# Kernel tuning notes

Measured on AMD Instinct MI355X. Metric: run time of the kernel, lower is better.

## Reference

```python
import jax, jax.numpy as jnp
import numpy as np

B, S, E, H = 4, 1024, 1024, 16
D = E // H  # head_dim = 64
SCALE = float(np.sqrt(D))


def setup_inputs() -> dict:
    key = jax.random.key(0)
    ks = jax.random.split(key, 12)
    lim = 1.0 / np.sqrt(E)  # torch nn.Linear default init range

    def lin(kw, kb):
        W = jax.random.uniform(kw, (E, E), jnp.float32, -lim, lim)
        b = jax.random.uniform(kb, (E,), jnp.float32, -lim, lim)
        return W, b

    W0, b0 = lin(ks[0], ks[1])
    W1, b1 = lin(ks[2], ks[3])
    W2, b2 = lin(ks[4], ks[5])
    Wv, bv = lin(ks[6], ks[7])
    Wo, bo = lin(ks[8], ks[9])
    A = jax.random.normal(ks[10], (D, D, D), jnp.float32)  # torch.randn core tensor
    x = jax.random.normal(ks[11], (B, S, E), jnp.float32)
    return {"x": x, "W0": W0, "b0": b0, "W1": W1, "b1": b1, "W2": W2, "b2": b2,
            "Wv": Wv, "bv": bv, "Wo": Wo, "bo": bo, "A": A}


def _heads(h):
    # (B,S,E) -> (B,H,S,D)
    return h.reshape(B, S, H, D).transpose(0, 2, 1, 3)


def reference(x, W0, b0, W1, b1, W2, b2, Wv, bv, Wo, bo, A):
    p0 = _heads(x @ W0.T + b0)
    p1 = _heads(x @ W1.T + b1)
    p2 = _heads(x @ W2.T + b2)
    # N=3 multilinear attention score: third projection is contracted over its
    # own sequence index k (faithful to the original einsum construction).
    logits = jnp.einsum('acd,bhia,bhjc,bhkd->bhij', A, p0, p1, p2,
                        optimize=True) / SCALE  # (B,H,S,S)
    attn = jax.nn.softmax(logits, axis=-1)  # dropout inactive (eval / p=0)
    v = _heads(x @ Wv.T + bv)
    values = jnp.einsum('bhij,bhjd->bhid', attn, v)  # (B,H,S,D)
    values = values.transpose(0, 2, 1, 3).reshape(B, S, E)
    out = values @ Wo.T + bo
    return out, attn
```

## Files before the change

kernel.cpp:

```cpp
#include <hip/hip_runtime.h>
#include <hip/hip_bf16.h>
#include <cstddef>

#define B_ 4
#define S_ 1024
#define E_ 1024
#define H_ 16
#define D_ 64
#define BH_ (B_*H_)

typedef __attribute__((ext_vector_type(8))) short short8;
typedef __attribute__((ext_vector_type(4))) float f32x4;
typedef __attribute__((ext_vector_type(4))) unsigned short us4;
typedef unsigned short u16;

__device__ inline u16 f2b(float x) {
    return __builtin_bit_cast(u16, __float2bfloat16(x));
}
__device__ inline float b2f(u16 u) {
    return __bfloat162float(__builtin_bit_cast(__hip_bfloat16, u));
}
__device__ inline void splitf(float x, u16& h, u16& l) {
    h = f2b(x); l = f2b(x - b2f(h));
}

__device__ inline void split_one(const float* __restrict__ in,
                                 u16* __restrict__ oh, u16* __restrict__ ol, int i)
{
    float4 v = ((const float4*)in)[i];
    us4 h, l;
    splitf(v.x, ((u16*)&h)[0], ((u16*)&l)[0]);
    splitf(v.y, ((u16*)&h)[1], ((u16*)&l)[1]);
    splitf(v.z, ((u16*)&h)[2], ((u16*)&l)[2]);
    splitf(v.w, ((u16*)&h)[3], ((u16*)&l)[3]);
    ((us4*)oh)[i] = h;
    ((us4*)ol)[i] = l;
}

__device__ inline void conv_one(const float* __restrict__ in,
                                u16* __restrict__ ob, int i)
{
    float4 v = ((const float4*)in)[i];
    us4 h;
    ((u16*)&h)[0] = f2b(v.x); ((u16*)&h)[1] = f2b(v.y);
    ((u16*)&h)[2] = f2b(v.z); ((u16*)&h)[3] = f2b(v.w);
    ((us4*)ob)[i] = h;
}

__global__ __launch_bounds__(256) void prep(
    const float* __restrict__ x, const float* __restrict__ W0,
    const float* __restrict__ W1, const float* __restrict__ Wv,
    const float* __restrict__ Wo, float* __restrict__ xsum_p,
    u16* __restrict__ xh, u16* __restrict__ xl,
    u16* __restrict__ w0h, u16* __restrict__ w0l,
    u16* __restrict__ w1h, u16* __restrict__ w1l,
    u16* __restrict__ wvb, u16* __restrict__ wob)
{
    int bid = blockIdx.x, tid = threadIdx.x;
    if (bid < 4096) {
        split_one(x, xh, xl, bid * 256 + tid);
    } else if (bid < 5120) {
        split_one(W0, w0h, w0l, (bid - 4096) * 256 + tid);
    } else if (bid < 6144) {
        split_one(W1, w1h, w1l, (bid - 5120) * 256 + tid);
    } else if (bid < 7168) {
        conv_one(Wv, wvb, (bid - 6144) * 256 + tid);
    } else if (bid < 8192) {
        conv_one(Wo, wob, (bid - 7168) * 256 + tid);
    } else {
        int p = bid - 8192;
        int kb = p & 3, b = (p >> 2) & 3, ch = p >> 4;
        int k = kb * 256 + tid;
        const float* base = x + ((size_t)(b * S_ + ch * 64)) * E_ + k;
        float s = 0.f;
#pragma unroll 8
        for (int j = 0; j < 64; ++j) s += base[(size_t)j * E_];
        xsum_p[(ch * 4 + b) * E_ + k] = s;
    }
}

__global__ __launch_bounds__(256) void t2k_M(
    const float* __restrict__ W2, const float* __restrict__ b2v,
    const float* __restrict__ xsum_p, const float* __restrict__ A,
    u16* __restrict__ MTh, u16* __restrict__ MTl)
{
    int h = blockIdx.x, b = blockIdx.y, tid = threadIdx.x;
    __shared__ float xs[1024];
    __shared__ float t2s[64];

#pragma unroll
    for (int j = 0; j < 4; ++j) {
        int k = j * 256 + tid;
        float s = 0.f;
#pragma unroll
        for (int c = 0; c < 16; ++c) s += xsum_p[(c * 4 + b) * E_ + k];
        xs[k] = s;
    }
    __syncthreads();

    int w = tid >> 6, lane = tid & 63;
    for (int nn = w; nn < 64; nn += 4) {
        int n = h * 64 + nn;
        const float* wr = W2 + (size_t)n * E_;
        float s = 0.f;
#pragma unroll
        for (int t = 0; t < 16; ++t) s = fmaf(wr[t * 64 + lane], xs[t * 64 + lane], s);
#pragma unroll
        for (int off = 1; off < 64; off <<= 1) s += __shfl_xor(s, off, 64);
        if (lane == 0) t2s[nn] = s + 1024.0f * b2v[n];
    }
    __syncthreads();

    int bh = b * H_ + h;
    int c = tid & 63;
    int a0 = (tid >> 6) * 16;
    for (int a = a0; a < a0 + 16; ++a) {
        float s = 0.f;
        const float* Ap = A + ((size_t)a * 64 + c) * 64;
#pragma unroll 8
        for (int d = 0; d < 64; ++d) s = fmaf(Ap[d], t2s[d], s);
        u16 hh, ll; splitf(s * 0.125f, hh, ll);
        MTh[(size_t)bh * 4096 + c * 64 + a] = hh;
        MTl[(size_t)bh * 4096 + c * 64 + a] = ll;
    }
}

__device__ void qp1_body(
    const u16* __restrict__ Xh, const u16* __restrict__ Xl,
    const u16* __restrict__ W0h_, const u16* __restrict__ W0l_,
    const u16* __restrict__ W1h_, const u16* __restrict__ W1l_,
    const float* __restrict__ bias0, const float* __restrict__ bias1,
    const u16* __restrict__ MTh, const u16* __restrict__ MTl,
    u16* __restrict__ qh, u16* __restrict__ ql,
    u16* __restrict__ p1h, u16* __restrict__ p1l,
    int bm, int bn, char* smem)
{
    const int K = 1024;
    u16* Xs_h  = (u16*)smem;
    u16* Xs_l  = Xs_h + 128 * 40;
    u16* W0s_h = Xs_l + 128 * 40;
    u16* W0s_l = W0s_h + 64 * 40;
    u16* W1s_h = W0s_l + 64 * 40;
    u16* W1s_l = W1s_h + 64 * 40;
    u16* Cs_h  = (u16*)smem;
    u16* Cs_l  = Cs_h + 128 * 72;

    const int tid = threadIdx.x;
    const int w = tid >> 6, lane = tid & 63;
    const int waveM = w & 1, waveN = w >> 1;
    const int quad = lane >> 4, l16 = lane & 15;

    const int xrow = tid >> 1, xko = (tid & 1) * 16;
    const int wrow = tid >> 2, wko = (tid & 3) * 8;

    const u16* xh_g  = Xh  + (size_t)(bm * 128 + xrow) * K + xko;
    const u16* xl_g  = Xl  + (size_t)(bm * 128 + xrow) * K + xko;
    const u16* w0h_g = W0h_ + (size_t)(bn * 64 + wrow) * K + wko;
    const u16* w0l_g = W0l_ + (size_t)(bn * 64 + wrow) * K + wko;
    const u16* w1h_g = W1h_ + (size_t)(bn * 64 + wrow) * K + wko;
    const u16* w1l_g = W1l_ + (size_t)(bn * 64 + wrow) * K + wko;

    f32x4 acc0[4][2] = {};
    f32x4 acc1[4][2] = {};

    for (int k0 = 0; k0 < K; k0 += 32) {
        uint4 xa = *(const uint4*)(xh_g + k0);
        uint4 xb = *(const uint4*)(xh_g + k0 + 8);
        uint4 xc = *(const uint4*)(xl_g + k0);
        uint4 xd = *(const uint4*)(xl_g + k0 + 8);
        uint4 w0a = *(const uint4*)(w0h_g + k0);
        uint4 w0c = *(const uint4*)(w0l_g + k0);
        uint4 w1a = *(const uint4*)(w1h_g + k0);
        uint4 w1c = *(const uint4*)(w1l_g + k0);
        __syncthreads();
        *(uint4*)&Xs_h[xrow * 40 + xko]     = xa;
        *(uint4*)&Xs_h[xrow * 40 + xko + 8] = xb;
        *(uint4*)&Xs_l[xrow * 40 + xko]     = xc;
        *(uint4*)&Xs_l[xrow * 40 + xko + 8] = xd;
        *(uint4*)&W0s_h[wrow * 40 + wko] = w0a;
        *(uint4*)&W0s_l[wrow * 40 + wko] = w0c;
        *(uint4*)&W1s_h[wrow * 40 + wko] = w1a;
        *(uint4*)&W1s_l[wrow * 40 + wko] = w1c;
        __syncthreads();

        short8 ah[4], al[4], b0h[2], b0l[2], b1h[2], b1l[2];
#pragma unroll
        for (int mt = 0; mt < 4; ++mt) {
            int r = (waveM * 64 + mt * 16 + l16) * 40 + quad * 8;
            ah[mt] = *(short8*)&Xs_h[r];
            al[mt] = *(short8*)&Xs_l[r];
        }
#pragma unroll
        for (int nt = 0; nt < 2; ++nt) {
            int r = (waveN * 32 + nt * 16 + l16) * 40 + quad * 8;
            b0h[nt] = *(short8*)&W0s_h[r];
            b0l[nt] = *(short8*)&W0s_l[r];
            b1h[nt] = *(short8*)&W1s_h[r];
            b1l[nt] = *(short8*)&W1s_l[r];
        }
#pragma unroll
        for (int mt = 0; mt < 4; ++mt)
#pragma unroll
            for (int nt = 0; nt < 2; ++nt) {
                acc0[mt][nt] = __builtin_amdgcn_mfma_f32_16x16x32_bf16(ah[mt], b0h[nt], acc0[mt][nt], 0, 0, 0);
                acc1[mt][nt] = __builtin_amdgcn_mfma_f32_16x16x32_bf16(ah[mt], b1h[nt], acc1[mt][nt], 0, 0, 0);
                acc0[mt][nt] = __builtin_amdgcn_mfma_f32_16x16x32_bf16(ah[mt], b0l[nt], acc0[mt][nt], 0, 0, 0);
                acc1[mt][nt] = __builtin_amdgcn_mfma_f32_16x16x32_bf16(ah[mt], b1l[nt], acc1[mt][nt], 0, 0, 0);
                acc0[mt][nt] = __builtin_amdgcn_mfma_f32_16x16x32_bf16(al[mt], b0h[nt], acc0[mt][nt], 0, 0, 0);
                acc1[mt][nt] = __builtin_amdgcn_mfma_f32_16x16x32_bf16(al[mt], b1h[nt], acc1[mt][nt], 0, 0, 0);
            }
    }

    const int bh = (bm >> 3) * H_ + bn;

#pragma unroll
    for (int mt = 0; mt < 4; ++mt)
#pragma unroll
        for (int nt = 0; nt < 2; ++nt)
#pragma unroll
            for (int r = 0; r < 4; ++r) {
                int m = bm * 128 + waveM * 64 + mt * 16 + quad * 4 + r;
                int n = bn * 64 + waveN * 32 + nt * 16 + l16;
                float val = acc1[mt][nt][r] + bias1[n];
                int s = m & 1023, c = n & 63;
                size_t addr = ((size_t)bh * S_ + s) * 64 + c;
                u16 hh, ll; splitf(val, hh, ll);
                p1h[addr] = hh; p1l[addr] = ll;
            }

    __syncthreads();
#pragma unroll
    for (int mt = 0; mt < 4; ++mt)
#pragma unroll
        for (int nt = 0; nt < 2; ++nt)
#pragma unroll
            for (int r = 0; r < 4; ++r) {
                int i = waveM * 64 + mt * 16 + quad * 4 + r;
                int a = waveN * 32 + nt * 16 + l16;
                float val = acc0[mt][nt][r] + bias0[bn * 64 + a];
                u16 hh, ll; splitf(val, hh, ll);
                Cs_h[i * 72 + a] = hh;
                Cs_l[i * 72 + a] = ll;
            }
    __syncthreads();

    const u16* MTh_b = MTh + (size_t)bh * 4096;
    const u16* MTl_b = MTl + (size_t)bh * 4096;
    f32x4 qacc[4][2] = {};
#pragma unroll
    for (int ch = 0; ch < 2; ++ch) {
        short8 mh[2], ml[2];
#pragma unroll
        for (int nt = 0; nt < 2; ++nt) {
            int c = waveN * 32 + nt * 16 + l16;
            mh[nt] = *(const short8*)&MTh_b[c * 64 + ch * 32 + quad * 8];
            ml[nt] = *(const short8*)&MTl_b[c * 64 + ch * 32 + quad * 8];
        }
#pragma unroll
        for (int mt = 0; mt < 4; ++mt) {
            int rr = (waveM * 64 + mt * 16 + l16) * 72 + ch * 32 + quad * 8;
            short8 ca = *(short8*)&Cs_h[rr];
            short8 cl = *(short8*)&Cs_l[rr];
#pragma unroll
            for (int nt = 0; nt < 2; ++nt) {
                qacc[mt][nt] = __builtin_amdgcn_mfma_f32_16x16x32_bf16(ca, mh[nt], qacc[mt][nt], 0, 0, 0);
                qacc[mt][nt] = __builtin_amdgcn_mfma_f32_16x16x32_bf16(ca, ml[nt], qacc[mt][nt], 0, 0, 0);
                qacc[mt][nt] = __builtin_amdgcn_mfma_f32_16x16x32_bf16(cl, mh[nt], qacc[mt][nt], 0, 0, 0);
            }
        }
    }
#pragma unroll
    for (int mt = 0; mt < 4; ++mt)
#pragma unroll
        for (int nt = 0; nt < 2; ++nt)
#pragma unroll
            for (int r = 0; r < 4; ++r) {
                int s = (bm & 7) * 128 + waveM * 64 + mt * 16 + quad * 4 + r;
                int c = waveN * 32 + nt * 16 + l16;
                size_t addr = ((size_t)bh * S_ + s) * 64 + c;
                u16 hh, ll; splitf(qacc[mt][nt][r], hh, ll);
                qh[addr] = hh; ql[addr] = ll;
            }
}

__device__ void plain128_body(
    const u16* __restrict__ Xb, const u16* __restrict__ Wb,
    const float* __restrict__ bias, u16* __restrict__ outB,
    float* __restrict__ outF, int mode, int bm, int bn, char* smem)
{
    const int K = 1024;
    u16* Xs = (u16*)smem;
    u16* Ws = Xs + 128 * 40;

    const int tid = threadIdx.x;
    const int w = tid >> 6, lane = tid & 63;
    const int waveM = w & 1, waveN = w >> 1;
    const int quad = lane >> 4, l16 = lane & 15;
    const int row = tid >> 1, ko = (tid & 1) * 16;

    const u16* xg = Xb + (size_t)(bm * 128 + row) * K + ko;
    const u16* wg = Wb + (size_t)(bn * 128 + row) * K + ko;

    f32x4 acc[4][4] = {};

    for (int k0 = 0; k0 < K; k0 += 32) {
        uint4 xa = *(const uint4*)(xg + k0);
        uint4 xb = *(const uint4*)(xg + k0 + 8);
        uint4 wa = *(const uint4*)(wg + k0);
        uint4 wb = *(const uint4*)(wg + k0 + 8);
        __syncthreads();
        *(uint4*)&Xs[row * 40 + ko]     = xa;
        *(uint4*)&Xs[row * 40 + ko + 8] = xb;
        *(uint4*)&Ws[row * 40 + ko]     = wa;
        *(uint4*)&Ws[row * 40 + ko + 8] = wb;
        __syncthreads();

        short8 af[4], bf_[4];
#pragma unroll
        for (int mt = 0; mt < 4; ++mt)
            af[mt] = *(short8*)&Xs[(waveM * 64 + mt * 16 + l16) * 40 + quad * 8];
#pragma unroll
        for (int nt = 0; nt < 4; ++nt)
            bf_[nt] = *(short8*)&Ws[(waveN * 64 + nt * 16 + l16) * 40 + quad * 8];
#pragma unroll
        for (int mt = 0; mt < 4; ++mt)
#pragma unroll
            for (int nt = 0; nt < 4; ++nt)
                acc[mt][nt] = __builtin_amdgcn_mfma_f32_16x16x32_bf16(af[mt], bf_[nt], acc[mt][nt], 0, 0, 0);
    }

#pragma unroll
    for (int mt = 0; mt < 4; ++mt)
#pragma unroll
        for (int nt = 0; nt < 4; ++nt)
#pragma unroll
            for (int r = 0; r < 4; ++r) {
                int m = bm * 128 + waveM * 64 + mt * 16 + quad * 4 + r;
                int n = bn * 128 + waveN * 64 + nt * 16 + l16;
                float val = acc[mt][nt][r] + bias[n];
                if (mode == 0) {
                    int b = m >> 10, s = m & 1023, h = n >> 6, c = n & 63;
                    outB[((size_t)((b * H_ + h) * 64 + c)) * S_ + s] = f2b(val);
                } else {
                    outF[(size_t)m * 1024 + n] = val;
                }
            }
}

__global__ __launch_bounds__(256) void gemm_mid(
    const u16* __restrict__ xh, const u16* __restrict__ xl,
    const u16* __restrict__ w0h, const u16* __restrict__ w0l,
    const u16* __restrict__ w1h, const u16* __restrict__ w1l,
    const float* __restrict__ b0, const float* __restrict__ b1,
    const u16* __restrict__ MTh, const u16* __restrict__ MTl,
    u16* __restrict__ qh, u16* __restrict__ ql,
    u16* __restrict__ p1h, u16* __restrict__ p1l,
    const u16* __restrict__ wvb, const float* __restrict__ bv,
    u16* __restrict__ vT)
{
    __shared__ __align__(16) char smem[40960];
    int bid = blockIdx.x;
    if (bid < 512) {
        qp1_body(xh, xl, w0h, w0l, w1h, w1l, b0, b1, MTh, MTl,
                 qh, ql, p1h, p1l, bid & 31, bid >> 5, smem);
    } else {
        int b2 = bid - 512;
        plain128_body(xh, wvb, bv, vT, nullptr, 0, b2 & 31, b2 >> 5, smem);
    }
}

__global__ __launch_bounds__(256) void gemm_fin(
    const u16* __restrict__ values, const u16* __restrict__ wob,
    const float* __restrict__ bo, float* __restrict__ out)
{
    __shared__ __align__(16) char smem[20480];
    plain128_body(values, wob, bo, nullptr, out, 1, blockIdx.x, blockIdx.y, smem);
}

__global__ __launch_bounds__(512) void logits_softmax_pv(
    const u16* __restrict__ qh, const u16* __restrict__ ql,
    const u16* __restrict__ p1h, const u16* __restrict__ p1l,
    const u16* __restrict__ vT, float* __restrict__ attn,
    u16* __restrict__ values)
{
    int bh = blockIdx.x, i0 = blockIdx.y * 32;
    int b = bh >> 4, h = bh & 15;
    int tid = threadIdx.x, w = tid >> 6, lane = tid & 63;
    int quad = lane >> 4, l16 = lane & 15;
    int wg = w >> 2, wj = w & 3;

    __shared__ __align__(16) char sm[56320];
    u16* qhs  = (u16*)sm;
    u16* qls  = (u16*)(sm + 4608);
    u16* p1hs = (u16*)(sm + 9216);
    u16* p1ls = (u16*)(sm + 27648);
    float* redm = (float*)(sm + 55296);
    float* reds = (float*)(sm + 55808);
    u16* Ps  = (u16*)sm;
    u16* vs_ = (u16*)(sm + 18432);

    {
        int row = tid >> 4, c0 = (tid & 15) * 4;
        size_t g = ((size_t)bh * S_ + i0 + row) * 64 + c0;
        *(us4*)&qhs[row * 72 + c0] = *(const us4*)&qh[g];
        *(us4*)&qls[row * 72 + c0] = *(const us4*)&ql[g];
    }

    const int jl = tid >> 3, c0s = (tid & 7) * 8;
    const size_t gp = ((size_t)bh * S_ + jl) * 64 + c0s;

    uint4 rha = *(const uint4*)&p1h[gp];
    uint4 rla = *(const uint4*)&p1l[gp];
    *(uint4*)&p1hs[jl * 72 + c0s] = rha;
    *(uint4*)&p1ls[jl * 72 + c0s] = rla;
    uint4 rh1 = *(const uint4*)&p1h[gp + 4096];
    uint4 rl1 = *(const uint4*)&p1l[gp + 4096];
    __syncthreads();

    short8 ah[2], al[2];
#pragma unroll
    for (int ch = 0; ch < 2; ++ch) {
        ah[ch] = *(short8*)&qhs[(wg * 16 + l16) * 72 + ch * 32 + quad * 8];
        al[ch] = *(short8*)&qls[(wg * 16 + l16) * 72 + ch * 32 + quad * 8];
    }

    f32x4 L[16];
    for (int t = 0; t < 16; ++t) {
        int cur = t & 1;
        uint4 rh2, rl2;
        if (t < 14) {
            size_t gn = gp + (size_t)(t + 2) * 4096;
            rh2 = *(const uint4*)&p1h[gn];
            rl2 = *(const uint4*)&p1l[gn];
        }
        int jr = wj * 16 + l16;
        const u16* Hb = &p1hs[cur * 4608 + jr * 72];
        const u16* Lb = &p1ls[cur * 4608 + jr * 72];
        short8 bh0 = *(const short8*)(Hb + quad * 8);
        short8 bh1 = *(const short8*)(Hb + 32 + quad * 8);
        short8 bl0 = *(const short8*)(Lb + quad * 8);
        short8 bl1 = *(const short8*)(Lb + 32 + quad * 8);
        f32x4 a = {};
        a = __builtin_amdgcn_mfma_f32_16x16x32_bf16(ah[0], bh0, a, 0, 0, 0);
        a = __builtin_amdgcn_mfma_f32_16x16x32_bf16(ah[1], bh1, a, 0, 0, 0);
        a = __builtin_amdgcn_mfma_f32_16x16x32_bf16(ah[0], bl0, a, 0, 0, 0);
        a = __builtin_amdgcn_mfma_f32_16x16x32_bf16(ah[1], bl1, a, 0, 0, 0);
        a = __builtin_amdgcn_mfma_f32_16x16x32_bf16(al[0], bh0, a, 0, 0, 0);
        a = __builtin_amdgcn_mfma_f32_16x16x32_bf16(al[1], bh1, a, 0, 0, 0);
        L[t] = a;
        if (t < 15) {
            *(uint4*)&p1hs[(1 - cur) * 4608 + jl * 72 + c0s] = rh1;
            *(uint4*)&p1ls[(1 - cur) * 4608 + jl * 72 + c0s] = rl1;
            if (t < 14) { rh1 = rh2; rl1 = rl2; }
            __syncthreads();
        }
    }

    float mrow[4], srow[4];
#pragma unroll
    for (int r = 0; r < 4; ++r) {
        float m = L[0][r];
#pragma unroll
        for (int t = 1; t < 16; ++t) m = fmaxf(m, L[t][r]);
#pragma unroll
        for (int off = 1; off < 16; off <<= 1) m = fmaxf(m, __shfl_xor(m, off, 64));
        mrow[r] = m;
    }
    if (l16 == 0)
#pragma unroll
        for (int r = 0; r < 4; ++r) redm[wj * 32 + wg * 16 + quad * 4 + r] = mrow[r];
    __syncthreads();
#pragma unroll
    for (int r = 0; r < 4; ++r) {
        int rowg = wg * 16 + quad * 4 + r;
        float m = fmaxf(fmaxf(redm[0 * 32 + rowg], redm[1 * 32 + rowg]),
                        fmaxf(redm[2 * 32 + rowg], redm[3 * 32 + rowg]));
        float s = 0.f;
#pragma unroll
        for (int t = 0; t < 16; ++t) { L[t][r] = __expf(L[t][r] - m); s += L[t][r]; }
#pragma unroll
        for (int off = 1; off < 16; off <<= 1) s += __shfl_xor(s, off, 64);
        srow[r] = s;
    }
    if (l16 == 0)
#pragma unroll
        for (int r = 0; r < 4; ++r) reds[wj * 32 + wg * 16 + quad * 4 + r] = srow[r];
    __syncthreads();
#pragma unroll
    for (int r = 0; r < 4; ++r) {
        int rowg = wg * 16 + quad * 4 + r;
        float inv = 1.0f / (reds[0 * 32 + rowg] + reds[1 * 32 + rowg] +
                            reds[2 * 32 + rowg] + reds[3 * 32 + rowg]);
        float* arow = attn + ((size_t)bh * S_ + i0 + rowg) * S_;
#pragma unroll
        for (int t = 0; t < 16; ++t) {
            float p = L[t][r] * inv;
            L[t][r] = p;
            __builtin_nontemporal_store(p, &arow[t * 64 + wj * 16 + l16]);
        }
    }

    const int dv = tid >> 3, jc = (tid & 7) * 8;
    const size_t gv = (size_t)(bh * 64 + dv) * S_;
    uint4 rv0 = *(const uint4*)&vT[gv + jc];
    uint4 rv1 = *(const uint4*)&vT[gv + 64 + jc];

    f32x4 acc_pv = {};
    const int d = wj * 16 + l16;
    for (int tt = 0; tt < 8; ++tt) {
        int cur = tt & 1;
        u16* Pb = Ps + cur * 4608;
        u16* Vb = vs_ + cur * 9216;
#pragma unroll
        for (int r = 0; r < 4; ++r) {
            int pr = (wg * 16 + quad * 4 + r) * 72 + wj * 16 + l16;
            Pb[pr]        = f2b(L[2 * tt][r]);
            Pb[2304 + pr] = f2b(L[2 * tt + 1][r]);
        }
        *(uint4*)&Vb[dv * 72 + jc]        = rv0;
        *(uint4*)&Vb[4608 + dv * 72 + jc] = rv1;
        __syncthreads();
        if (tt < 7) {
            rv0 = *(const uint4*)&vT[gv + (size_t)(2 * tt + 2) * 64 + jc];
            rv1 = *(const uint4*)&vT[gv + (size_t)(2 * tt + 3) * 64 + jc];
        }
#pragma unroll
        for (int tp = 0; tp < 2; ++tp)
#pragma unroll
            for (int cc = 0; cc < 64; cc += 32) {
                short8 af = *(short8*)&Pb[tp * 2304 + (wg * 16 + l16) * 72 + cc + quad * 8];
                short8 bf = *(short8*)&vs_[cur * 9216 + tp * 4608 + d * 72 + cc + quad * 8];
                acc_pv = __builtin_amdgcn_mfma_f32_16x16x32_bf16(af, bf, acc_pv, 0, 0, 0);
            }
    }
#pragma unroll
    for (int r = 0; r < 4; ++r) {
        int i = i0 + wg * 16 + quad * 4 + r;
        values[((size_t)(b * S_ + i)) * E_ + h * 64 + d] = f2b(acc_pv[r]);
    }
}

extern "C" void kernel_launch(void* const* d_in, const int* in_sizes, int n_in,
                              void* d_out, int out_size, void* d_ws, size_t ws_size,
                              hipStream_t stream)
{
    const float* x  = (const float*)d_in[0];
    const float* W0 = (const float*)d_in[1];
    const float* b0 = (const float*)d_in[2];
    const float* W1 = (const float*)d_in[3];
    const float* b1 = (const float*)d_in[4];
    const float* W2 = (const float*)d_in[5];
    const float* b2 = (const float*)d_in[6];
    const float* Wv = (const float*)d_in[7];
    const float* bv = (const float*)d_in[8];
    const float* Wo = (const float*)d_in[9];
    const float* bo = (const float*)d_in[10];
    const float* A  = (const float*)d_in[11];

    float* out  = (float*)d_out;
    float* attn = out + (size_t)B_ * S_ * E_;

    u16* xh  = (u16*)d_ws;
    u16* xl  = xh + 4194304;
    u16* w0h = xl + 4194304;
    u16* w0l = w0h + 1048576;
    u16* w1h = w0l + 1048576;
    u16* w1l = w1h + 1048576;
    u16* p1h = w1l + 1048576;
    u16* p1l = p1h + 4194304;
    u16* qh  = p1l + 4194304;
    u16* ql  = qh + 4194304;
    u16* vT  = ql + 4194304;
    u16* values = vT + 4194304;
    u16* MTh = values + 4194304;
    u16* MTl = MTh + 262144;
    u16* wob = MTl + 262144;
    float* xsum_p = (float*)p1h;
    u16* wvb = values;

    prep<<<8448, 256, 0, stream>>>(x, W0, W1, Wv, Wo, xsum_p,
                                   xh, xl, w0h, w0l, w1h, w1l, wvb, wob);
    t2k_M<<<dim3(16, 4), 256, 0, stream>>>(W2, b2, xsum_p, A, MTh, MTl);

    gemm_mid<<<768, 256, 0, stream>>>(xh, xl, w0h, w0l, w1h, w1l,
                                      b0, b1, MTh, MTl, qh, ql, p1h, p1l,
                                      wvb, bv, vT);

    logits_softmax_pv<<<dim3(64, 32), 512, 0, stream>>>(qh, ql, p1h, p1l, vT, attn, values);

    gemm_fin<<<dim3(32, 8), 256, 0, stream>>>(values, wob, bo, out);
}
```

Before: 542.7 us.

## Load Q fragments directly to registers, swizzle PV LDS, remap mid-GEMM blocks

The attention kernel now loads its Q hi/lo fragments straight from global memory into registers instead of staging them through LDS. The P and V shared buffers switch from padded rows (stride 72) to an XOR-swizzled stride of 64. Together these shrink the LDS footprint from about 55 KB to 48 KB, which may allow more resident blocks, while keeping bank conflicts low. The mid GEMM also interleaves block IDs so the qp1 and V-projection blocks are mixed across the dispatch order, at the risk of worse cache locality between neighbouring blocks.

Measured after the change: 600.8 us. 1.11x slower.

```diff
diff --git a/kernel.cpp b/kernel.cpp
--- a/kernel.cpp
+++ b/kernel.cpp
@@ -359,7 +359,8 @@
     u16* __restrict__ vT)
 {
     __shared__ __align__(16) char smem[40960];
-    int bid = blockIdx.x;
+    int bid0 = blockIdx.x;
+    int bid = (bid0 & 7) * 96 + (bid0 >> 3);
     if (bid < 512) {
         qp1_body(xh, xl, w0h, w0l, w1h, w1l, b0, b1, MTh, MTl,
                  qh, ql, p1h, p1l, bid & 31, bid >> 5, smem);
@@ -389,21 +390,21 @@
     int quad = lane >> 4, l16 = lane & 15;
     int wg = w >> 2, wj = w & 3;
 
-    __shared__ __align__(16) char sm[56320];
-    u16* qhs  = (u16*)sm;
-    u16* qls  = (u16*)(sm + 4608);
-    u16* p1hs = (u16*)(sm + 9216);
-    u16* p1ls = (u16*)(sm + 27648);
-    float* redm = (float*)(sm + 55296);
-    float* reds = (float*)(sm + 55808);
+    __shared__ __align__(16) char sm[49152];
+    u16* p1hs = (u16*)sm;
+    u16* p1ls = (u16*)(sm + 18432);
+    float* redm = (float*)(sm + 36864);
+    float* reds = (float*)(sm + 37376);
     u16* Ps  = (u16*)sm;
-    u16* vs_ = (u16*)(sm + 18432);
-
+    u16* vs_ = (u16*)(sm + 16384);
+
+    short8 ah[2], al[2];
     {
-        int row = tid >> 4, c0 = (tid & 15) * 4;
-        size_t g = ((size_t)bh * S_ + i0 + row) * 64 + c0;
-        *(us4*)&qhs[row * 72 + c0] = *(const us4*)&qh[g];
-        *(us4*)&qls[row * 72 + c0] = *(const us4*)&ql[g];
+        size_t gq = ((size_t)bh * S_ + i0 + wg * 16 + l16) * 64 + quad * 8;
+        ah[0] = *(const short8*)&qh[gq];
+        ah[1] = *(const short8*)&qh[gq + 32];
+        al[0] = *(const short8*)&ql[gq];
+        al[1] = *(const short8*)&ql[gq + 32];
     }
 
     const int jl = tid >> 3, c0s = (tid & 7) * 8;
@@ -416,13 +417,6 @@
     uint4 rh1 = *(const uint4*)&p1h[gp + 4096];
     uint4 rl1 = *(const uint4*)&p1l[gp + 4096];
     __syncthreads();
-
-    short8 ah[2], al[2];
-#pragma unroll
-    for (int ch = 0; ch < 2; ++ch) {
-        ah[ch] = *(short8*)&qhs[(wg * 16 + l16) * 72 + ch * 32 + quad * 8];
-        al[ch] = *(short8*)&qls[(wg * 16 + l16) * 72 + ch * 32 + quad * 8];
-    }
 
     f32x4 L[16];
     for (int t = 0; t < 16; ++t) {
@@ -507,18 +501,23 @@
 
     f32x4 acc_pv = {};
     const int d = wj * 16 + l16;
+    const int vwsw = (dv * 64 + jc) ^ ((dv & 7) << 3);
+    const int prow_rd = wg * 16 + l16;
+    const int vrow_sw = (d & 7) << 3;
+    const int prow_sw = (prow_rd & 7) << 3;
     for (int tt = 0; tt < 8; ++tt) {
         int cur = tt & 1;
-        u16* Pb = Ps + cur * 4608;
-        u16* Vb = vs_ + cur * 9216;
+        u16* Pb = Ps + cur * 4096;
+        u16* Vb = vs_ + cur * 8192;
 #pragma unroll
         for (int r = 0; r < 4; ++r) {
-            int pr = (wg * 16 + quad * 4 + r) * 72 + wj * 16 + l16;
-            Pb[pr]        = f2b(L[2 * tt][r]);
-            Pb[2304 + pr] = f2b(L[2 * tt + 1][r]);
-        }
-        *(uint4*)&Vb[dv * 72 + jc]        = rv0;
-        *(uint4*)&Vb[4608 + dv * 72 + jc] = rv1;
+            int prow = wg * 16 + quad * 4 + r;
+            int pidx = ((prow * 64 + wj * 16 + l16)) ^ ((prow & 7) << 3);
+            Pb[pidx]        = f2b(L[2 * tt][r]);
+            Pb[2048 + pidx] = f2b(L[2 * tt + 1][r]);
+        }
+        *(uint4*)&Vb[vwsw]        = rv0;
+        *(uint4*)&Vb[4096 + vwsw] = rv1;
         __syncthreads();
         if (tt < 7) {
             rv0 = *(const uint4*)&vT[gv + (size_t)(2 * tt + 2) * 64 + jc];
@@ -528,8 +527,8 @@
         for (int tp = 0; tp < 2; ++tp)
 #pragma unroll
             for (int cc = 0; cc < 64; cc += 32) {
-                short8 af = *(short8*)&Pb[tp * 2304 + (wg * 16 + l16) * 72 + cc + quad * 8];
-                short8 bf = *(short8*)&vs_[cur * 9216 + tp * 4608 + d * 72 + cc + quad * 8];
+                short8 af = *(short8*)&Pb[tp * 2048 + ((prow_rd * 64 + cc + quad * 8) ^ prow_sw)];
+                short8 bf = *(short8*)&Vb[tp * 4096 + ((d * 64 + cc + quad * 8) ^ vrow_sw)];
                 acc_pv = __builtin_amdgcn_mfma_f32_16x16x32_bf16(af, bf, acc_pv, 0, 0, 0);
             }
     }
```
